# Kernel tuning notes

Measured on AMD Instinct MI355X. Metric: run time of the kernel, lower is better.

Reference implementation:

```python
import jax, jax.numpy as jnp
import numpy as np

EPS = 1e-08

def setup_inputs() -> dict:
    key = jax.random.key(0)
    k1, k2, k3 = jax.random.split(key, 3)
    B, N, D = 8192, 64, 256
    query_embs = jax.random.normal(k1, (B, D), dtype=jnp.float32)
    support_embs = jax.random.normal(k2, (B, N, D), dtype=jnp.float32)
    labels = jax.random.randint(k3, (B, N), 0, 2, dtype=jnp.int32)
    return {"query_embs": query_embs, "support_embs": support_embs, "labels": labels}

def reference(query_embs, support_embs, labels):
    # mask: (B, N) float, 1 where label == 1
    mask = (labels == 1).astype(support_embs.dtype)
    count = jnp.sum(mask, axis=1)  # (B,)
    # masked sum over support dim -> (B, D)
    proto_sum = jnp.einsum('bn,bnd->bd', mask, support_embs)
    proto_mean = proto_sum / jnp.maximum(count, 1.0)[:, None]
    # fallback: if no positives, use support_embs[b, 0]
    prototypes = jnp.where((count > 0)[:, None], proto_mean, support_embs[:, 0, :])
    diff = query_embs - prototypes  # (B, D)
    distances = jnp.sqrt(jnp.sum(diff * diff, axis=1) + EPS)  # (B,)
    return jnp.mean(distances)
```

## Files before the change

### kernel.cpp

```cpp
#include <hip/hip_runtime.h>
#include <math.h>


__global__ __launch_bounds__(256) void proto_dist_kernel(
    const float* __restrict__ query,
    const float* __restrict__ support,
    const int*   __restrict__ labels,
    float* __restrict__ dists,
    int B)
{
    const int lane = threadIdx.x & 63;
    const int wv   = threadIdx.x >> 6;
    const int b    = blockIdx.x * 4 + wv;
    if (b >= B) return;

    const float4 q = ((const float4*)(query + (size_t)b * 256))[lane];

    const int lab = labels[(size_t)b * 64 + lane];
    const unsigned long long m = __ballot(lab == 1);
    const int count = __popcll(m);

    const float4* srow = (const float4*)(support + (size_t)b * 64 * 256);

    float4 acc = make_float4(0.f, 0.f, 0.f, 0.f);
    unsigned long long mm = m;
    while (mm) {
        int   n[8];
        float w[8];
        n[0] = __builtin_ctzll(mm);
        w[0] = 1.0f;
        mm &= (mm - 1ULL);
        #pragma unroll
        for (int j = 1; j < 8; ++j) {
            const bool has = (mm != 0ULL);
            n[j] = has ? __builtin_ctzll(mm) : n[0];
            w[j] = has ? 1.0f : 0.0f;
            mm   = has ? (mm & (mm - 1ULL)) : 0ULL;
        }
        float4 v[8];
        #pragma unroll
        for (int j = 0; j < 8; ++j)
            v[j] = srow[(size_t)n[j] * 64 + lane];
        #pragma unroll
        for (int j = 0; j < 8; ++j) {
            acc.x = fmaf(w[j], v[j].x, acc.x);
            acc.y = fmaf(w[j], v[j].y, acc.y);
            acc.z = fmaf(w[j], v[j].z, acc.z);
            acc.w = fmaf(w[j], v[j].w, acc.w);
        }
    }

    float4 proto;
    if (count > 0) {
        const float inv = 1.0f / (float)count;
        proto = make_float4(acc.x * inv, acc.y * inv, acc.z * inv, acc.w * inv);
    } else {
        proto = srow[lane];
    }

    const float dx = q.x - proto.x;
    const float dy = q.y - proto.y;
    const float dz = q.z - proto.z;
    const float dw = q.w - proto.w;
    float ss = dx * dx + dy * dy + dz * dz + dw * dw;

    #pragma unroll
    for (int off = 32; off > 0; off >>= 1)
        ss += __shfl_down(ss, off, 64);

    if (lane == 0)
        dists[b] = sqrtf(ss + 1e-8f);
}

__global__ __launch_bounds__(256) void reduce_mean_kernel(
    const float* __restrict__ dists, float* __restrict__ out, int B)
{
    __shared__ float sm[4];
    float s = 0.f;
    for (int i = threadIdx.x; i < B; i += 256)
        s += dists[i];
    #pragma unroll
    for (int off = 32; off > 0; off >>= 1)
        s += __shfl_down(s, off, 64);
    const int lane = threadIdx.x & 63;
    const int wv   = threadIdx.x >> 6;
    if (lane == 0) sm[wv] = s;
    __syncthreads();
    if (threadIdx.x == 0)
        out[0] = (sm[0] + sm[1] + sm[2] + sm[3]) / (float)B;
}

extern "C" void kernel_launch(void* const* d_in, const int* in_sizes, int n_in,
                              void* d_out, int out_size, void* d_ws, size_t ws_size,
                              hipStream_t stream) {
    const float* query   = (const float*)d_in[0];
    const float* support = (const float*)d_in[1];
    const int*   labels  = (const int*)d_in[2];
    float* out = (float*)d_out;

    const int n_q = in_sizes[0];
    const int n_s = in_sizes[1];
    const int n_l = in_sizes[2];
    const int D = n_s / n_l;
    const int B = n_q / D;
    (void)n_in; (void)out_size; (void)ws_size;

    float* dists = (float*)d_ws;

    const int blocks = (B + 3) / 4;
    proto_dist_kernel<<<blocks, 256, 0, stream>>>(query, support, labels, dists, B);
    reduce_mean_kernel<<<1, 256, 0, stream>>>(dists, out, B);
}
```

Before: 639.1 us.

## Split each batch row across four waves with dense masked row loads

Each block now handles one batch element, and its four waves each accumulate 16 support rows. Every row is loaded unconditionally and weighted by its mask bit, replacing the serial ctz-driven gather of only the positive rows. Partial sums are combined through shared memory before wave 0 computes the distance. This aims to raise memory-level parallelism and remove the serial bit-scanning loop, at the cost of reading all support rows (roughly twice the bytes) and adding a block barrier.

```diff
diff --git a/kernel.cpp b/kernel.cpp
--- a/kernel.cpp
+++ b/kernel.cpp
@@ -11,10 +11,10 @@
 {
     const int lane = threadIdx.x & 63;
     const int wv   = threadIdx.x >> 6;
-    const int b    = blockIdx.x * 4 + wv;
+    const int b    = blockIdx.x;
     if (b >= B) return;
 
-    const float4 q = ((const float4*)(query + (size_t)b * 256))[lane];
+    __shared__ float4 part[4][64];
 
     const int lab = labels[(size_t)b * 64 + lane];
     const unsigned long long m = __ballot(lab == 1);
@@ -22,54 +22,54 @@
 
     const float4* srow = (const float4*)(support + (size_t)b * 64 * 256);
 
+    float4 q = make_float4(0.f, 0.f, 0.f, 0.f);
+    if (wv == 0)
+        q = ((const float4*)(query + (size_t)b * 256))[lane];
+
+    const int r0 = wv * 16;
     float4 acc = make_float4(0.f, 0.f, 0.f, 0.f);
-    unsigned long long mm = m;
-    while (mm) {
-        int   n[8];
-        float w[8];
-        n[0] = __builtin_ctzll(mm);
-        w[0] = 1.0f;
-        mm &= (mm - 1ULL);
+    #pragma unroll
+    for (int j = 0; j < 16; ++j) {
+        const float  w = ((m >> (unsigned)(r0 + j)) & 1ULL) ? 1.0f : 0.0f;
+        const float4 v = srow[(size_t)(r0 + j) * 64 + lane];
+        acc.x = fmaf(w, v.x, acc.x);
+        acc.y = fmaf(w, v.y, acc.y);
+        acc.z = fmaf(w, v.z, acc.z);
+        acc.w = fmaf(w, v.w, acc.w);
+    }
+    part[wv][lane] = acc;
+    __syncthreads();
+
+    if (wv == 0) {
+        const float4 s0 = part[0][lane];
+        const float4 s1 = part[1][lane];
+        const float4 s2 = part[2][lane];
+        const float4 s3 = part[3][lane];
+        float4 sum = make_float4(s0.x + s1.x + s2.x + s3.x,
+                                 s0.y + s1.y + s2.y + s3.y,
+                                 s0.z + s1.z + s2.z + s3.z,
+                                 s0.w + s1.w + s2.w + s3.w);
+        float4 proto;
+        if (count > 0) {
+            const float inv = 1.0f / (float)count;
+            proto = make_float4(sum.x * inv, sum.y * inv, sum.z * inv, sum.w * inv);
+        } else {
+            proto = srow[lane];
+        }
+
+        const float dx = q.x - proto.x;
+        const float dy = q.y - proto.y;
+        const float dz = q.z - proto.z;
+        const float dw = q.w - proto.w;
+        float ss = dx * dx + dy * dy + dz * dz + dw * dw;
+
         #pragma unroll
-        for (int j = 1; j < 8; ++j) {
-            const bool has = (mm != 0ULL);
-            n[j] = has ? __builtin_ctzll(mm) : n[0];
-            w[j] = has ? 1.0f : 0.0f;
-            mm   = has ? (mm & (mm - 1ULL)) : 0ULL;
-        }
-        float4 v[8];
-        #pragma unroll
-        for (int j = 0; j < 8; ++j)
-            v[j] = srow[(size_t)n[j] * 64 + lane];
-        #pragma unroll
-        for (int j = 0; j < 8; ++j) {
-            acc.x = fmaf(w[j], v[j].x, acc.x);
-            acc.y = fmaf(w[j], v[j].y, acc.y);
-            acc.z = fmaf(w[j], v[j].z, acc.z);
-            acc.w = fmaf(w[j], v[j].w, acc.w);
-        }
+        for (int off = 32; off > 0; off >>= 1)
+            ss += __shfl_down(ss, off, 64);
+
+        if (lane == 0)
+            dists[b] = sqrtf(ss + 1e-8f);
     }
-
-    float4 proto;
-    if (count > 0) {
-        const float inv = 1.0f / (float)count;
-        proto = make_float4(acc.x * inv, acc.y * inv, acc.z * inv, acc.w * inv);
-    } else {
-        proto = srow[lane];
-    }
-
-    const float dx = q.x - proto.x;
-    const float dy = q.y - proto.y;
-    const float dz = q.z - proto.z;
-    const float dw = q.w - proto.w;
-    float ss = dx * dx + dy * dy + dz * dz + dw * dw;
-
-    #pragma unroll
-    for (int off = 32; off > 0; off >>= 1)
-        ss += __shfl_down(ss, off, 64);
-
-    if (lane == 0)
-        dists[b] = sqrtf(ss + 1e-8f);
 }
 
 __global__ __launch_bounds__(256) void reduce_mean_kernel(
@@ -107,7 +107,6 @@
 
     float* dists = (float*)d_ws;
 
-    const int blocks = (B + 3) / 4;
-    proto_dist_kernel<<<blocks, 256, 0, stream>>>(query, support, labels, dists, B);
+    proto_dist_kernel<<<B, 256, 0, stream>>>(query, support, labels, dists, B);
     reduce_mean_kernel<<<1, 256, 0, stream>>>(dists, out, B);
 }
```

After: 686.4 us. 7.4% more time.
